# Kernel optimization log

Measured on AMD Instinct MI355X. Metric: run time of the kernel, lower is better.

Reference implementation:

```python
import jax, jax.numpy as jnp
import numpy as np
from jax.scipy.special import logsumexp

S, D, K, R, P = 500, 768, 16, 256, 64  # seq_len, bert_dim, out_dim, n_pairs, max wordpieces/entity


def setup_inputs() -> dict:
    key = jax.random.key(0)
    k1, k2, k3, k4, k5, k6 = jax.random.split(key, 6)
    word_embeddings = jax.random.normal(k1, (S, D), jnp.float32)
    # kaiming_normal_ fan_in = D*K (last two dims collapsed); gain sqrt(2) for relu
    W = jax.random.normal(k2, (D, K, D), jnp.float32) * np.float32((2.0 / (K * D)) ** 0.5)
    idx1 = jax.random.randint(k3, (R, P), 0, S)
    idx2 = jax.random.randint(k4, (R, P), 0, S)
    # ragged mention lengths -> padding masks (at least 1 valid wordpiece)
    len1 = jax.random.randint(k5, (R,), 1, P + 1)
    len2 = jax.random.randint(k6, (R,), 1, P + 1)
    pos = jnp.arange(P)
    mask1 = (pos[None, :] < len1[:, None]).astype(jnp.float32)
    mask2 = (pos[None, :] < len2[:, None]).astype(jnp.float32)
    return {"word_embeddings": word_embeddings, "W": W, "idx1": idx1, "idx2": idx2,
            "mask1": mask1, "mask2": mask2}


def reference(word_embeddings, W, idx1, idx2, mask1, mask2):
    # gather ragged mention wordpieces (padded to P per entity)
    e1 = word_embeddings[idx1]  # [R, P, D]
    e2 = word_embeddings[idx2]  # [R, P, D]
    # biaffine: z[r,k,p,q] = e1[r,p,:] @ W[:,k,:] @ e2[r,q,:]
    zh = jnp.einsum('rpd,dke->rpke', e1, W)      # [R, P, K, D]
    z = jnp.einsum('rpke,rqe->rkpq', zh, e2)     # [R, K, P, P]
    # logsumexp pooling over all valid (p, q) mention-token pairs
    b = mask1[:, None, :, None] * mask2[:, None, None, :]  # [R, 1, P, P]
    scores = logsumexp(z, axis=(2, 3), b=b)      # [R, K]
    return scores
```

## Files before the change

### kernel.cpp

```cpp
#include <hip/hip_runtime.h>
#include <math.h>

#define S_ 500
#define D_ 768
#define K_ 16
#define R_ 256
#define P_ 64
#define NT 12

typedef unsigned short ushort_t;
typedef __attribute__((ext_vector_type(8))) short short8;
typedef __attribute__((ext_vector_type(4))) float floatx4;
typedef __attribute__((ext_vector_type(4))) float fx4;

__device__ inline ushort_t f2bf(float x) {
  unsigned int u = __float_as_uint(x);
  u += 0x7fffu + ((u >> 16) & 1u);
  return (ushort_t)(u >> 16);
}

__device__ inline unsigned int cvtpk(float lo, float hi) {
  unsigned int r;
  asm("v_cvt_pk_bf16_f32 %0, %1, %2" : "=v"(r) : "v"(lo), "v"(hi));
  return r;
}

#define GLD_LDS16(g, l)                                                        \
  __builtin_amdgcn_global_load_lds(                                            \
      (const __attribute__((address_space(1))) void*)(g),                      \
      (__attribute__((address_space(3))) void*)(l), 16, 0, 0)

#define ASM_BARRIER asm volatile("s_barrier" ::: "memory")
#define WAIT_VM6 asm volatile("s_waitcnt vmcnt(6)" ::: "memory")
#define WAIT_VM0 asm volatile("s_waitcnt vmcnt(0)" ::: "memory")

__global__ __launch_bounds__(256) void prep(const float* __restrict__ WE,
                                            ushort_t* __restrict__ WEb) {
  const int t = threadIdx.x;
  int gid = blockIdx.x * 256 + t;
  int row = gid / 192;
  ushort4 o = {0, 0, 0, 0};
  if (row < S_) {
    float4 v = *(const float4*)(WE + (size_t)gid * 4);
    o.x = f2bf(v.x); o.y = f2bf(v.y); o.z = f2bf(v.z); o.w = f2bf(v.w);
  }
  *(ushort4*)(WEb + (size_t)gid * 4) = o;
}

__global__ __launch_bounds__(256, 2) void mm0_fused(const ushort_t* __restrict__ A,
                                                    const float* __restrict__ Wf,
                                                    ushort_t* __restrict__ C) {
  __shared__ ushort_t As[2][2][128 * 32];
  __shared__ ushort_t Bs[2][2][128 * 32];
  const int tid = threadIdx.x;
  const int wave = tid >> 6, lane = tid & 63;
  const int m0 = blockIdx.y * 128, n0 = blockIdx.x * 128;
  const int wm = (wave & 1) * 64, wn = (wave >> 1) * 64;
  const int col = lane & 15, quad = lane >> 4;

  floatx4 acc[4][4];
#pragma unroll
  for (int i = 0; i < 4; i++)
#pragma unroll
    for (int j = 0; j < 4; j++)
#pragma unroll
      for (int e = 0; e < 4; e++) acc[i][j][e] = 0.f;

  const int srow = wave * 32 + (lane >> 2);
  const int scol = (lane & 3) * 8;
  const ushort_t* ga0 = A + (size_t)(m0 + srow) * D_ + scol;
  const int ldsbase = (wave * 32) * 32;

#define ISSUE_A(t_, buf_)                                                      \
  do {                                                                         \
    const ushort_t* ga = ga0 + (t_)*64;                                        \
    GLD_LDS16(ga, &As[buf_][0][ldsbase]);                                      \
    GLD_LDS16(ga + 16 * D_, &As[buf_][0][ldsbase + 16 * 32]);                  \
    GLD_LDS16(ga + 32, &As[buf_][1][ldsbase]);                                 \
    GLD_LDS16(ga + 32 + 16 * D_, &As[buf_][1][ldsbase + 16 * 32]);             \
  } while (0)

  const int nq = tid & 31;
  const int dqA = tid >> 5;
  const float* gwA = Wf + (size_t)(dqA * 4) * 12288 + n0 + nq * 4;
  const float* gwB = gwA + (size_t)32 * 12288;

  fx4 bv[2][4];
#define LOADB(t_)                                                              \
  do {                                                                         \
    _Pragma("unroll") for (int i = 0; i < 4; i++) {                            \
      bv[0][i] = *(const fx4*)(gwA + (size_t)((t_)*64 + i) * 12288);           \
      bv[1][i] = *(const fx4*)(gwB + (size_t)((t_)*64 + i) * 12288);           \
    }                                                                          \
  } while (0)

#define WRITEB(buf_)                                                           \
  do {                                                                         \
    _Pragma("unroll") for (int h = 0; h < 2; h++)                              \
    _Pragma("unroll") for (int j = 0; j < 4; j++) {                            \
      int row = nq * 4 + j;                                                    \
      uint2 w;                                                                 \
      w.x = cvtpk(bv[h][0][j], bv[h][1][j]);                                   \
      w.y = cvtpk(bv[h][2][j], bv[h][3][j]);                                   \
      *(uint2*)((char*)&Bs[buf_][h][0] +                                       \
                ((row * 64 + dqA * 8) ^ ((nq & 15) << 4))) = w;                \
    }                                                                          \
  } while (0)

  ISSUE_A(0, 0);
  LOADB(0);
  for (int t = 0; t < NT; ++t) {
    const int cur = t & 1;
    WRITEB(cur);
    __syncthreads();
    if (t + 1 < NT) {
      ISSUE_A(t + 1, cur ^ 1);
      LOADB(t + 1);
    }
#pragma unroll
    for (int s = 0; s < 2; ++s) {
      short8 a[4], b[4];
#pragma unroll
      for (int i = 0; i < 4; i++)
        a[i] = *(const short8*)&As[cur][s][(wm + i * 16 + col) * 32 + quad * 8];
#pragma unroll
      for (int j = 0; j < 4; j++) {
        int row = wn + j * 16 + col;
        b[j] = *(const short8*)((const char*)&Bs[cur][s][0] +
                                ((row * 64 + quad * 16) ^ (((row >> 2) & 15) << 4)));
      }
#pragma unroll
      for (int i = 0; i < 4; i++)
#pragma unroll
        for (int j = 0; j < 4; j++)
          acc[i][j] = __builtin_amdgcn_mfma_f32_16x16x32_bf16(b[j], a[i], acc[i][j], 0, 0, 0);
    }
  }
#undef ISSUE_A
#undef LOADB
#undef WRITEB

#pragma unroll
  for (int i = 0; i < 4; i++) {
    int m = m0 + wm + i * 16 + col;
#pragma unroll
    for (int j = 0; j < 4; j++) {
      int n = n0 + wn + j * 16 + quad * 4;
      ushort4 o;
      o.x = f2bf(acc[i][j][0]); o.y = f2bf(acc[i][j][1]);
      o.z = f2bf(acc[i][j][2]); o.w = f2bf(acc[i][j][3]);
      *(ushort4*)(C + (size_t)m * 12288 + n) = o;
    }
  }
}

__global__ __launch_bounds__(256, 2) void mm1_bt(const ushort_t* __restrict__ A,
                                                 const ushort_t* __restrict__ Bm,
                                                 ushort_t* __restrict__ G) {
  __shared__ ushort_t As[2][2][128 * 32];
  __shared__ ushort_t Bs[2][2][64 * 32];
  const int tid = threadIdx.x;
  const int wave = tid >> 6, lane = tid & 63;
  const int lin = blockIdx.x + (blockIdx.y << 3);
  const int yb = ((lin & 7) << 3) | (lin >> 6);
  const int xb = (lin >> 3) & 7;
  const int m0 = yb * 128, n0 = xb * 64;
  const int wm = (wave & 1) * 64, wn = (wave >> 1) * 32;
  const int col = lane & 15, quad = lane >> 4;

  floatx4 acc[4][2];
#pragma unroll
  for (int i = 0; i < 4; i++)
#pragma unroll
    for (int j = 0; j < 2; j++)
#pragma unroll
      for (int e = 0; e < 4; e++) acc[i][j][e] = 0.f;

  const int lrow = lane >> 2, scol = (lane & 3) * 8;
  const ushort_t* ga0 = A + (size_t)(m0 + wave * 32 + lrow) * D_ + scol;
  const ushort_t* gb0 = Bm + (size_t)(n0 + wave * 16 + lrow) * D_ + scol;
  const int aoff = (wave * 32) * 32;
  const int boff = (wave * 16) * 32;

#define ISSUE_TILE1(t_, buf_)                                                  \
  do {                                                                         \
    _Pragma("unroll") for (int s_ = 0; s_ < 2; s_++) {                         \
      const ushort_t* ga = ga0 + (t_)*64 + s_ * 32;                            \
      const ushort_t* gb = gb0 + (t_)*64 + s_ * 32;                            \
      GLD_LDS16(ga, &As[buf_][s_][aoff]);                                      \
      GLD_LDS16(ga + 16 * D_, &As[buf_][s_][aoff + 16 * 32]);                  \
      GLD_LDS16(gb, &Bs[buf_][s_][boff]);                                      \
    }                                                                          \
  } while (0)

  ISSUE_TILE1(0, 0);
  for (int t = 0; t < NT; ++t) {
    const int cur = t & 1;
    if (t + 1 < NT) {
      ISSUE_TILE1(t + 1, cur ^ 1);
      WAIT_VM6;
    } else {
      WAIT_VM0;
    }
    ASM_BARRIER;
#pragma unroll
    for (int s = 0; s < 2; ++s) {
      short8 a[4], b[2];
#pragma unroll
      for (int i = 0; i < 4; i++)
        a[i] = *(const short8*)&As[cur][s][(wm + i * 16 + col) * 32 + quad * 8];
#pragma unroll
      for (int j = 0; j < 2; j++)
        b[j] = *(const short8*)&Bs[cur][s][(wn + j * 16 + col) * 32 + quad * 8];
#pragma unroll
      for (int i = 0; i < 4; i++)
#pragma unroll
        for (int j = 0; j < 2; j++)
          acc[i][j] = __builtin_amdgcn_mfma_f32_16x16x32_bf16(a[i], b[j], acc[i][j], 0, 0, 0);
    }
    ASM_BARRIER;
  }
#undef ISSUE_TILE1

#pragma unroll
  for (int i = 0; i < 4; i++) {
    int s1 = (m0 + wm + i * 16) >> 4;
#pragma unroll
    for (int j = 0; j < 2; j++) {
      int s2 = n0 + wn + j * 16 + col;
      if (s1 < S_ && s2 < S_) {
        ushort4 o;
        o.x = f2bf(acc[i][j][0]); o.y = f2bf(acc[i][j][1]);
        o.z = f2bf(acc[i][j][2]); o.w = f2bf(acc[i][j][3]);
        *(ushort4*)(G + (((size_t)s1 * S_ + s2) << 4) + quad * 4) = o;
      }
    }
  }
}

__global__ __launch_bounds__(512) void lse_kernel(const ushort_t* __restrict__ G,
                                                  const int* __restrict__ idx1,
                                                  const int* __restrict__ idx2,
                                                  const float* __restrict__ mask1,
                                                  const float* __restrict__ mask2,
                                                  float* __restrict__ out) {
  const int r = blockIdx.x;
  const int tid = threadIdx.x;
  __shared__ int b1[P_], b2[P_];
  __shared__ int s_len1, s_len2;
  __shared__ float wmx[8][K_], wsum[8][K_];

  if (tid < 64) {
    float mv = mask1[r * P_ + tid];
    unsigned long long bal = __ballot(mv > 0.5f);
    if (tid == 0) s_len1 = (int)__popcll(bal);
    b1[tid] = idx1[r * P_ + tid] * (S_ * K_);
  } else if (tid < 128) {
    int q = tid - 64;
    float mv = mask2[r * P_ + q];
    unsigned long long bal = __ballot(mv > 0.5f);
    if (q == 0) s_len2 = (int)__popcll(bal);
    b2[q] = idx2[r * P_ + q] * K_;
  }
  __syncthreads();
  const int len2 = s_len2;
  const int total = s_len1 * len2;

  float m[K_], s[K_];
#pragma unroll
  for (int k = 0; k < K_; k++) { m[k] = -3.0e38f; s[k] = 0.f; }

  for (int i = tid; i < total; i += 512) {
    int p = i / len2;
    int q = i - p * len2;
    const uint4* g4 = (const uint4*)(G + b1[p] + b2[q]);
    uint4 w0 = g4[0], w1 = g4[1];
    unsigned int uu[8] = {w0.x, w0.y, w0.z, w0.w, w1.x, w1.y, w1.z, w1.w};
    float z[K_];
#pragma unroll
    for (int h = 0; h < 8; h++) {
      z[2 * h + 0] = __uint_as_float(uu[h] << 16);
      z[2 * h + 1] = __uint_as_float(uu[h] & 0xffff0000u);
    }
#pragma unroll
    for (int k = 0; k < K_; k++) {
      float d = z[k] - m[k];
      float e = __expf(-fabsf(d));
      bool up = d > 0.f;
      s[k] = up ? __fmaf_rn(s[k], e, 1.f) : (s[k] + e);
      m[k] = up ? z[k] : m[k];
    }
  }

#pragma unroll
  for (int off = 1; off < 64; off <<= 1) {
#pragma unroll
    for (int k = 0; k < K_; k++) {
      float mo = __shfl_xor(m[k], off, 64);
      float so = __shfl_xor(s[k], off, 64);
      float d = mo - m[k];
      float e = __expf(-fabsf(d));
      bool up = d > 0.f;
      s[k] = up ? __fmaf_rn(s[k], e, so) : __fmaf_rn(so, e, s[k]);
      m[k] = up ? mo : m[k];
    }
  }
  const int wave = tid >> 6, lane = tid & 63;
  if (lane == 0) {
#pragma unroll
    for (int k = 0; k < K_; k++) { wmx[wave][k] = m[k]; wsum[wave][k] = s[k]; }
  }
  __syncthreads();
  if (tid < K_) {
    float M = -3.0e38f, Ssum = 0.f;
#pragma unroll
    for (int w = 0; w < 8; w++) {
      float mo = wmx[w][tid], so = wsum[w][tid];
      float d = mo - M;
      float e = __expf(-fabsf(d));
      bool up = d > 0.f;
      Ssum = up ? __fmaf_rn(Ssum, e, so) : __fmaf_rn(so, e, Ssum);
      M = up ? mo : M;
    }
    out[r * K_ + tid] = M + __logf(Ssum);
  }
}

extern "C" void kernel_launch(void* const* d_in, const int* in_sizes, int n_in,
                              void* d_out, int out_size, void* d_ws, size_t ws_size,
                              hipStream_t stream) {
  const float* WE    = (const float*)d_in[0];
  const float* W     = (const float*)d_in[1];
  const int*   idx1  = (const int*)d_in[2];
  const int*   idx2  = (const int*)d_in[3];
  const float* mask1 = (const float*)d_in[4];
  const float* mask2 = (const float*)d_in[5];
  float* out = (float*)d_out;

  ushort_t* WEb   = (ushort_t*)d_ws;
  ushort_t* projb = WEb + (size_t)512 * 768;
  ushort_t* G     = projb + (size_t)512 * 12288;

  prep<<<384, 256, 0, stream>>>(WE, WEb);
  mm0_fused<<<dim3(96, 4), 256, 0, stream>>>(WEb, W, projb);
  mm1_bt<<<dim3(8, 64), 256, 0, stream>>>(projb, WEb, G);
  lse_kernel<<<R_, 512, 0, stream>>>(G, idx1, idx2, mask1, mask2, out);
}
```

Baseline: 133.8 us.

## Halve mm0 N-tile to 64 and remap blocks for occupancy and locality

The first GEMM (embeddings × W reshaped to D×K·D) now uses 128×64 output tiles instead of 128×128. That doubles the grid to 768 blocks, and launch bounds allow 3 blocks per SM. Block indices are remapped so that consecutive blocks share W column tiles across the four M tiles, and the B-tile LDS swizzle and staging layout are changed to match. The goal is better CU fill and latency hiding for the fp32 W stream. The cost is lower per-block arithmetic intensity, because A is re-read twice as often, and more register pressure from the 3-block launch bound.

```diff
diff --git a/kernel.cpp b/kernel.cpp
--- a/kernel.cpp
+++ b/kernel.cpp
@@ -47,22 +47,25 @@
   *(ushort4*)(WEb + (size_t)gid * 4) = o;
 }
 
-__global__ __launch_bounds__(256, 2) void mm0_fused(const ushort_t* __restrict__ A,
+__global__ __launch_bounds__(256, 3) void mm0_fused(const ushort_t* __restrict__ A,
                                                     const float* __restrict__ Wf,
                                                     ushort_t* __restrict__ C) {
   __shared__ ushort_t As[2][2][128 * 32];
-  __shared__ ushort_t Bs[2][2][128 * 32];
+  __shared__ ushort_t Bs[2][2][64 * 32];
   const int tid = threadIdx.x;
   const int wave = tid >> 6, lane = tid & 63;
-  const int m0 = blockIdx.y * 128, n0 = blockIdx.x * 128;
-  const int wm = (wave & 1) * 64, wn = (wave >> 1) * 64;
+  const int lin = blockIdx.x + 192 * blockIdx.y;
+  const int qx = lin & 7, mi = lin >> 3;
+  const int xb = qx * 24 + (mi >> 2), yb = mi & 3;
+  const int m0 = yb * 128, n0 = xb * 64;
+  const int wm = (wave & 1) * 64, wn = (wave >> 1) * 32;
   const int col = lane & 15, quad = lane >> 4;
 
-  floatx4 acc[4][4];
+  floatx4 acc[4][2];
 #pragma unroll
   for (int i = 0; i < 4; i++)
 #pragma unroll
-    for (int j = 0; j < 4; j++)
+    for (int j = 0; j < 2; j++)
 #pragma unroll
       for (int e = 0; e < 4; e++) acc[i][j][e] = 0.f;
 
@@ -80,30 +83,28 @@
     GLD_LDS16(ga + 32 + 16 * D_, &As[buf_][1][ldsbase + 16 * 32]);             \
   } while (0)
 
-  const int nq = tid & 31;
-  const int dqA = tid >> 5;
-  const float* gwA = Wf + (size_t)(dqA * 4) * 12288 + n0 + nq * 4;
-  const float* gwB = gwA + (size_t)32 * 12288;
-
-  fx4 bv[2][4];
+  const int nq = tid & 15;
+  const int dqt = tid >> 4;
+  const int hB = dqt >> 3;
+  const int kqB = dqt & 7;
+  const float* gw = Wf + (size_t)(hB * 32 + kqB * 4) * 12288 + n0 + nq * 4;
+
+  fx4 bv[4];
 #define LOADB(t_)                                                              \
   do {                                                                         \
-    _Pragma("unroll") for (int i = 0; i < 4; i++) {                            \
-      bv[0][i] = *(const fx4*)(gwA + (size_t)((t_)*64 + i) * 12288);           \
-      bv[1][i] = *(const fx4*)(gwB + (size_t)((t_)*64 + i) * 12288);           \
-    }                                                                          \
+    _Pragma("unroll") for (int i = 0; i < 4; i++)                              \
+        bv[i] = *(const fx4*)(gw + (size_t)((t_)*64 + i) * 12288);             \
   } while (0)
 
 #define WRITEB(buf_)                                                           \
   do {                                                                         \
-    _Pragma("unroll") for (int h = 0; h < 2; h++)                              \
     _Pragma("unroll") for (int j = 0; j < 4; j++) {                            \
       int row = nq * 4 + j;                                                    \
       uint2 w;                                                                 \
-      w.x = cvtpk(bv[h][0][j], bv[h][1][j]);                                   \
-      w.y = cvtpk(bv[h][2][j], bv[h][3][j]);                                   \
-      *(uint2*)((char*)&Bs[buf_][h][0] +                                       \
-                ((row * 64 + dqA * 8) ^ ((nq & 15) << 4))) = w;                \
+      w.x = cvtpk(bv[0][j], bv[1][j]);                                         \
+      w.y = cvtpk(bv[2][j], bv[3][j]);                                         \
+      *(uint2*)((char*)&Bs[buf_][hB][0] +                                      \
+                ((row * 64 + kqB * 8) ^ ((row & 3) << 4))) = w;                \
     }                                                                          \
   } while (0)
 
@@ -119,20 +120,20 @@
     }
 #pragma unroll
     for (int s = 0; s < 2; ++s) {
-      short8 a[4], b[4];
+      short8 a[4], b[2];
 #pragma unroll
       for (int i = 0; i < 4; i++)
         a[i] = *(const short8*)&As[cur][s][(wm + i * 16 + col) * 32 + quad * 8];
 #pragma unroll
-      for (int j = 0; j < 4; j++) {
+      for (int j = 0; j < 2; j++) {
         int row = wn + j * 16 + col;
         b[j] = *(const short8*)((const char*)&Bs[cur][s][0] +
-                                ((row * 64 + quad * 16) ^ (((row >> 2) & 15) << 4)));
+                                ((row * 64 + quad * 16) ^ ((row & 3) << 4)));
       }
 #pragma unroll
       for (int i = 0; i < 4; i++)
 #pragma unroll
-        for (int j = 0; j < 4; j++)
+        for (int j = 0; j < 2; j++)
           acc[i][j] = __builtin_amdgcn_mfma_f32_16x16x32_bf16(b[j], a[i], acc[i][j], 0, 0, 0);
     }
   }
@@ -144,7 +145,7 @@
   for (int i = 0; i < 4; i++) {
     int m = m0 + wm + i * 16 + col;
 #pragma unroll
-    for (int j = 0; j < 4; j++) {
+    for (int j = 0; j < 2; j++) {
       int n = n0 + wn + j * 16 + quad * 4;
       ushort4 o;
       o.x = f2bf(acc[i][j][0]); o.y = f2bf(acc[i][j][1]);
@@ -342,7 +343,7 @@
   ushort_t* G     = projb + (size_t)512 * 12288;
 
   prep<<<384, 256, 0, stream>>>(WE, WEb);
-  mm0_fused<<<dim3(96, 4), 256, 0, stream>>>(WEb, W, projb);
+  mm0_fused<<<dim3(192, 4), 256, 0, stream>>>(WEb, W, projb);
   mm1_bt<<<dim3(8, 64), 256, 0, stream>>>(projb, WEb, G);
   lse_kernel<<<R_, 512, 0, stream>>>(G, idx1, idx2, mask1, mask2, out);
 }
```

New measurement: 142.6 us. +6.6%, slower.

## Fuse fp32-to-bf16 embedding conversion into both GEMM kernels, drop prep kernel

Applied to the files above, without the earlier changes.

Removes the separate prep kernel that converted word embeddings to bf16. Both GEMMs now load fp32 embeddings directly, convert them in registers and write swizzled bf16 into LDS. mm1 changes its pipelining from async global-to-LDS loads with explicit vmcnt waits to register staging with __syncthreads. This saves one launch and one round trip through memory, but adds conversion work and register pressure, and the mm1 loop may lose some overlap.

```diff
diff --git a/kernel.cpp b/kernel.cpp
--- a/kernel.cpp
+++ b/kernel.cpp
@@ -30,26 +30,9 @@
       (const __attribute__((address_space(1))) void*)(g),                      \
       (__attribute__((address_space(3))) void*)(l), 16, 0, 0)
 
-#define ASM_BARRIER asm volatile("s_barrier" ::: "memory")
-#define WAIT_VM6 asm volatile("s_waitcnt vmcnt(6)" ::: "memory")
-#define WAIT_VM0 asm volatile("s_waitcnt vmcnt(0)" ::: "memory")
-
-__global__ __launch_bounds__(256) void prep(const float* __restrict__ WE,
-                                            ushort_t* __restrict__ WEb) {
-  const int t = threadIdx.x;
-  int gid = blockIdx.x * 256 + t;
-  int row = gid / 192;
-  ushort4 o = {0, 0, 0, 0};
-  if (row < S_) {
-    float4 v = *(const float4*)(WE + (size_t)gid * 4);
-    o.x = f2bf(v.x); o.y = f2bf(v.y); o.z = f2bf(v.z); o.w = f2bf(v.w);
-  }
-  *(ushort4*)(WEb + (size_t)gid * 4) = o;
-}
-
-__global__ __launch_bounds__(256, 2) void mm0_fused(const ushort_t* __restrict__ A,
-                                                    const float* __restrict__ Wf,
-                                                    ushort_t* __restrict__ C) {
+__global__ __launch_bounds__(256, 2) void mm0_f(const float* __restrict__ WE,
+                                                const float* __restrict__ Wf,
+                                                ushort_t* __restrict__ C) {
   __shared__ ushort_t As[2][2][128 * 32];
   __shared__ ushort_t Bs[2][2][128 * 32];
   const int tid = threadIdx.x;
@@ -66,25 +49,35 @@
 #pragma unroll
       for (int e = 0; e < 4; e++) acc[i][j][e] = 0.f;
 
-  const int srow = wave * 32 + (lane >> 2);
-  const int scol = (lane & 3) * 8;
-  const ushort_t* ga0 = A + (size_t)(m0 + srow) * D_ + scol;
-  const int ldsbase = (wave * 32) * 32;
-
-#define ISSUE_A(t_, buf_)                                                      \
-  do {                                                                         \
-    const ushort_t* ga = ga0 + (t_)*64;                                        \
-    GLD_LDS16(ga, &As[buf_][0][ldsbase]);                                      \
-    GLD_LDS16(ga + 16 * D_, &As[buf_][0][ldsbase + 16 * 32]);                  \
-    GLD_LDS16(ga + 32, &As[buf_][1][ldsbase]);                                 \
-    GLD_LDS16(ga + 32 + 16 * D_, &As[buf_][1][ldsbase + 16 * 32]);             \
+  const int ra = tid >> 1, ka = tid & 1;
+  const bool va = (m0 + ra) < S_;
+  const fx4* wa = (const fx4*)WE + (size_t)(m0 + ra) * 192 + ka * 8;
+  fx4 av[8];
+#define LOADA(t_)                                                              \
+  do {                                                                         \
+    _Pragma("unroll") for (int i = 0; i < 8; i++) {                            \
+      if (va) av[i] = wa[(t_)*16 + i];                                         \
+      else { av[i][0] = 0.f; av[i][1] = 0.f; av[i][2] = 0.f; av[i][3] = 0.f; } \
+    }                                                                          \
+  } while (0)
+
+#define WRITEA(buf_)                                                           \
+  do {                                                                         \
+    _Pragma("unroll") for (int j = 0; j < 4; j++) {                            \
+      uint4 o;                                                                 \
+      o.x = cvtpk(av[2 * j][0], av[2 * j][1]);                                 \
+      o.y = cvtpk(av[2 * j][2], av[2 * j][3]);                                 \
+      o.z = cvtpk(av[2 * j + 1][0], av[2 * j + 1][1]);                         \
+      o.w = cvtpk(av[2 * j + 1][2], av[2 * j + 1][3]);                         \
+      *(uint4*)((char*)&As[buf_][ka][0] +                                      \
+                ((ra * 64 + j * 16) ^ ((ra & 15) << 4))) = o;                  \
+    }                                                                          \
   } while (0)
 
   const int nq = tid & 31;
   const int dqA = tid >> 5;
   const float* gwA = Wf + (size_t)(dqA * 4) * 12288 + n0 + nq * 4;
   const float* gwB = gwA + (size_t)32 * 12288;
-
   fx4 bv[2][4];
 #define LOADB(t_)                                                              \
   do {                                                                         \
@@ -107,22 +100,23 @@
     }                                                                          \
   } while (0)
 
-  ISSUE_A(0, 0);
+  LOADA(0);
   LOADB(0);
+  WRITEA(0);
+  WRITEB(0);
   for (int t = 0; t < NT; ++t) {
     const int cur = t & 1;
-    WRITEB(cur);
     __syncthreads();
-    if (t + 1 < NT) {
-      ISSUE_A(t + 1, cur ^ 1);
-      LOADB(t + 1);
-    }
+    if (t + 1 < NT) { LOADA(t + 1); LOADB(t + 1); }
 #pragma unroll
     for (int s = 0; s < 2; ++s) {
       short8 a[4], b[4];
 #pragma unroll
-      for (int i = 0; i < 4; i++)
-        a[i] = *(const short8*)&As[cur][s][(wm + i * 16 + col) * 32 + quad * 8];
+      for (int i = 0; i < 4; i++) {
+        int row = wm + i * 16 + col;
+        a[i] = *(const short8*)((const char*)&As[cur][s][0] +
+                                ((row * 64 + quad * 16) ^ (col << 4)));
+      }
 #pragma unroll
       for (int j = 0; j < 4; j++) {
         int row = wn + j * 16 + col;
@@ -135,8 +129,13 @@
         for (int j = 0; j < 4; j++)
           acc[i][j] = __builtin_amdgcn_mfma_f32_16x16x32_bf16(b[j], a[i], acc[i][j], 0, 0, 0);
     }
-  }
-#undef ISSUE_A
+    if (t + 1 < NT) {
+      WRITEA(cur ^ 1);
+      WRITEB(cur ^ 1);
+    }
+  }
+#undef LOADA
+#undef WRITEA
 #undef LOADB
 #undef WRITEB
 
@@ -154,9 +153,9 @@
   }
 }
 
-__global__ __launch_bounds__(256, 2) void mm1_bt(const ushort_t* __restrict__ A,
-                                                 const ushort_t* __restrict__ Bm,
-                                                 ushort_t* __restrict__ G) {
+__global__ __launch_bounds__(256, 2) void mm1_f(const ushort_t* __restrict__ A,
+                                                const float* __restrict__ WE,
+                                                ushort_t* __restrict__ G) {
   __shared__ ushort_t As[2][2][128 * 32];
   __shared__ ushort_t Bs[2][2][64 * 32];
   const int tid = threadIdx.x;
@@ -178,31 +177,50 @@
 
   const int lrow = lane >> 2, scol = (lane & 3) * 8;
   const ushort_t* ga0 = A + (size_t)(m0 + wave * 32 + lrow) * D_ + scol;
-  const ushort_t* gb0 = Bm + (size_t)(n0 + wave * 16 + lrow) * D_ + scol;
   const int aoff = (wave * 32) * 32;
-  const int boff = (wave * 16) * 32;
-
-#define ISSUE_TILE1(t_, buf_)                                                  \
+#define ISSUE_A1(t_, buf_)                                                     \
   do {                                                                         \
     _Pragma("unroll") for (int s_ = 0; s_ < 2; s_++) {                         \
       const ushort_t* ga = ga0 + (t_)*64 + s_ * 32;                            \
-      const ushort_t* gb = gb0 + (t_)*64 + s_ * 32;                            \
       GLD_LDS16(ga, &As[buf_][s_][aoff]);                                      \
       GLD_LDS16(ga + 16 * D_, &As[buf_][s_][aoff + 16 * 32]);                  \
-      GLD_LDS16(gb, &Bs[buf_][s_][boff]);                                      \
-    }                                                                          \
-  } while (0)
-
-  ISSUE_TILE1(0, 0);
+    }                                                                          \
+  } while (0)
+
+  const int rb = tid >> 2, kq = tid & 3;
+  const bool vb = (n0 + rb) < S_;
+  const fx4* wb = (const fx4*)WE + (size_t)(n0 + rb) * 192 + kq * 4;
+  fx4 bvv[4];
+#define LOADB1(t_)                                                             \
+  do {                                                                         \
+    _Pragma("unroll") for (int i = 0; i < 4; i++) {                            \
+      if (vb) bvv[i] = wb[(t_)*16 + i];                                        \
+      else { bvv[i][0]=0.f; bvv[i][1]=0.f; bvv[i][2]=0.f; bvv[i][3]=0.f; }     \
+    }                                                                          \
+  } while (0)
+
+#define WRITEB1(buf_)                                                          \
+  do {                                                                         \
+    uint4 u0, u1;                                                              \
+    u0.x = cvtpk(bvv[0][0], bvv[0][1]); u0.y = cvtpk(bvv[0][2], bvv[0][3]);    \
+    u0.z = cvtpk(bvv[1][0], bvv[1][1]); u0.w = cvtpk(bvv[1][2], bvv[1][3]);    \
+    u1.x = cvtpk(bvv[2][0], bvv[2][1]); u1.y = cvtpk(bvv[2][2], bvv[2][3]);    \
+    u1.z = cvtpk(bvv[3][0], bvv[3][1]); u1.w = cvtpk(bvv[3][2], bvv[3][3]);    \
+    char* bp = (char*)&Bs[buf_][kq >> 1][0] + rb * 64 + (kq & 1) * 32;         \
+    *(uint4*)bp = u0;                                                          \
+    *(uint4*)(bp + 16) = u1;                                                   \
+  } while (0)
+
+  LOADB1(0);
+  ISSUE_A1(0, 0);
+  WRITEB1(0);
   for (int t = 0; t < NT; ++t) {
     const int cur = t & 1;
+    __syncthreads();
     if (t + 1 < NT) {
-      ISSUE_TILE1(t + 1, cur ^ 1);
-      WAIT_VM6;
-    } else {
-      WAIT_VM0;
-    }
-    ASM_BARRIER;
+      LOADB1(t + 1);
+      ISSUE_A1(t + 1, cur ^ 1);
+    }
 #pragma unroll
     for (int s = 0; s < 2; ++s) {
       short8 a[4], b[2];
@@ -218,9 +236,12 @@
         for (int j = 0; j < 2; j++)
           acc[i][j] = __builtin_amdgcn_mfma_f32_16x16x32_bf16(a[i], b[j], acc[i][j], 0, 0, 0);
     }
-    ASM_BARRIER;
-  }
-#undef ISSUE_TILE1
+    if (t + 1 < NT)
+      WRITEB1(cur ^ 1);
+  }
+#undef ISSUE_A1
+#undef LOADB1
+#undef WRITEB1
 
 #pragma unroll
   for (int i = 0; i < 4; i++) {
@@ -330,19 +351,17 @@
                               void* d_out, int out_size, void* d_ws, size_t ws_size,
                               hipStream_t stream) {
   const float* WE    = (const float*)d_in[0];
-  const float* W     = (const float*)d_in[1];
+  const float* Wf    = (const float*)d_in[1];
   const int*   idx1  = (const int*)d_in[2];
   const int*   idx2  = (const int*)d_in[3];
   const float* mask1 = (const float*)d_in[4];
   const float* mask2 = (const float*)d_in[5];
   float* out = (float*)d_out;
 
-  ushort_t* WEb   = (ushort_t*)d_ws;
-  ushort_t* projb = WEb + (size_t)512 * 768;
+  ushort_t* projb = (ushort_t*)d_ws;
   ushort_t* G     = projb + (size_t)512 * 12288;
 
-  prep<<<384, 256, 0, stream>>>(WE, WEb);
-  mm0_fused<<<dim3(96, 4), 256, 0, stream>>>(WEb, W, projb);
-  mm1_bt<<<dim3(8, 64), 256, 0, stream>>>(projb, WEb, G);
+  mm0_f<<<dim3(96, 4), 256, 0, stream>>>(WE, Wf, projb);
+  mm1_f<<<dim3(8, 64), 256, 0, stream>>>(projb, WE, G);
   lse_kernel<<<R_, 512, 0, stream>>>(G, idx1, idx2, mask1, mask2, out);
 }
```

Result: slower. 155.8 us (+16.4%).
